# Kernel optimization log

Hardware: AMD Instinct MI355X
Metric: run time of the kernel (lower is better)

## Reference

```python
import jax, jax.numpy as jnp
import numpy as np

B, L, SH, EH, A, T = 128, 200, 512, 512, 512, 3


def setup_inputs() -> dict:
    key = jax.random.key(0)
    ks = jax.random.split(key, 13)
    s = 0.05  # small init scale to keep tanh/sigmoid unsaturated
    return {
        "sent_enc_doc": jax.random.normal(ks[0], (B, L, 2 * SH), jnp.float32),
        "h0_w": jax.random.normal(ks[1], (EH, SH), jnp.float32) * s,
        "h0_b": jax.random.normal(ks[2], (EH,), jnp.float32) * s,
        "gru_w_ih": jax.random.normal(ks[3], (3 * EH, 2 * SH), jnp.float32) * s,
        "gru_w_hh": jax.random.normal(ks[4], (3 * EH, EH), jnp.float32) * s,
        "gru_b_ih": jax.random.normal(ks[5], (3 * EH,), jnp.float32) * s,
        "gru_b_hh": jax.random.normal(ks[6], (3 * EH,), jnp.float32) * s,
        "wq": jax.random.normal(ks[7], (A, EH), jnp.float32) * s,
        "bq": jax.random.normal(ks[8], (A,), jnp.float32) * s,
        "wd": jax.random.normal(ks[9], (A, 2 * SH), jnp.float32) * s,
        "bd": jax.random.normal(ks[10], (A,), jnp.float32) * s,
        "ws": jax.random.normal(ks[11], (1, A), jnp.float32) * s,
        "bs": jax.random.normal(ks[12], (1,), jnp.float32) * s,
    }


def reference(sent_enc_doc, h0_w, h0_b, gru_w_ih, gru_w_hh, gru_b_ih, gru_b_hh,
              wq, bq, wd, bd, ws, bs):
    b, l, d2 = sent_enc_doc.shape
    sh = d2 // 2
    eh = gru_w_hh.shape[1]
    neg = jnp.asarray(-1e6, sent_enc_doc.dtype)

    # h0 = tanh(W * last backward vector), replicated across doc_len
    last_back = sent_enc_doc[:, 0, sh:]                      # (B, SH)
    h0 = jnp.tanh(last_back @ h0_w.T + h0_b)                 # (B, EH)
    h = jnp.broadcast_to(h0[:, None, :], (b, l, eh))         # (B, L, EH)

    s_prev = jnp.zeros((b, l, d2), sent_enc_doc.dtype)
    d_proj = sent_enc_doc @ wd.T + bd                        # (B, L, A) - loop-invariant
    mask = jnp.zeros((b, l), bool)
    rows = jnp.arange(b)

    scores_list, sel_list = [], []
    for _ in range(T):  # fixed, tiny, sequentially-dependent loop
        # GRUCell (torch gate order: r, z, n)
        gx = s_prev @ gru_w_ih.T + gru_b_ih                  # (B, L, 3EH)
        gh = h @ gru_w_hh.T + gru_b_hh                       # (B, L, 3EH)
        xr, xz, xn = jnp.split(gx, 3, axis=-1)
        hr, hz, hn = jnp.split(gh, 3, axis=-1)
        r = jax.nn.sigmoid(xr + hr)
        z = jax.nn.sigmoid(xz + hz)
        n = jnp.tanh(xn + r * hn)
        h = (1.0 - z) * n + z * h                            # (B, L, EH)

        # scorer: ws . tanh(Wq h + Wd s_i)
        score = (jnp.tanh(h @ wq.T + bq + d_proj) @ ws.T + bs)[..., 0]  # (B, L)
        score = jnp.where(mask, neg, score)
        idx = jnp.argmax(score, axis=1)                      # (B,)
        mask = mask.at[rows, idx].set(True)

        # gather the selected sentence encoding, broadcast to all positions
        s_sel = jnp.take_along_axis(sent_enc_doc, idx[:, None, None], axis=1)  # (B,1,2SH)
        s_prev = jnp.broadcast_to(s_sel, (b, l, d2))

        scores_list.append(score)
        sel_list.append(idx)

    sents_scores = jnp.stack(scores_list, axis=1)            # (B, T, L)
    sents_selected = jnp.stack(sel_list, axis=1)             # (B, T)
    return sents_scores, sents_selected
```

## Files before the change

kernel.cpp:

```cpp
#include <hip/hip_runtime.h>
#include <hip/hip_bf16.h>

constexpr int Bn  = 128;
constexpr int Ln  = 200;
constexpr int D2n = 1024;
constexpr int G3n = 1536;
constexpr int Tn  = 3;
constexpr int Nn  = 512;
constexpr int Kn  = 1024;

typedef unsigned short ushort;
typedef float f32x4 __attribute__((ext_vector_type(4)));
typedef __bf16 bf16x8 __attribute__((ext_vector_type(8)));

__device__ __forceinline__ ushort f2bf(float f) {
  unsigned u = __float_as_uint(f);
  unsigned r = (u + 0x7fffu + ((u >> 16) & 1u)) >> 16;
  return (ushort)r;
}
__device__ __forceinline__ float bf2f(ushort h) {
  return __uint_as_float(((unsigned)h) << 16);
}

__device__ __forceinline__ void gld_lds16(const ushort* g, ushort* l) {
  __builtin_amdgcn_global_load_lds(
      (const __attribute__((address_space(1))) unsigned int*)g,
      (__attribute__((address_space(3))) unsigned int*)l, 16, 0, 0);
}

__global__ void k_gather_lastb(const float* __restrict__ sent, float* __restrict__ lastb) {
  int i = blockIdx.x * 256 + threadIdx.x;
  int b = i >> 9, k = i & 511;
  lastb[i] = sent[(size_t)b * (Ln * D2n) + 512 + k];
}

__global__ void k_split(const float* __restrict__ W, ushort* __restrict__ hi,
                        ushort* __restrict__ lo) {
  int i = blockIdx.x * 256 + threadIdx.x;
  float4 v = ((const float4*)W)[i];
  ushort4 h, l;
  h.x = f2bf(v.x); l.x = f2bf(v.x - bf2f(h.x));
  h.y = f2bf(v.y); l.y = f2bf(v.y - bf2f(h.y));
  h.z = f2bf(v.z); l.z = f2bf(v.z - bf2f(h.z));
  h.w = f2bf(v.w); l.w = f2bf(v.w - bf2f(h.w));
  ((ushort4*)hi)[i] = h;
  ((ushort4*)lo)[i] = l;
}

template<int K, int ACT>
__launch_bounds__(256)
__global__ void k_small_gemm(const float* __restrict__ in, const float* __restrict__ W,
                             const float* __restrict__ bias, float* __restrict__ out, int J) {
  __shared__ float s[16 * K];
  const int b0 = blockIdx.y * 16;
  const int jl = threadIdx.x & 63;
  const int j  = blockIdx.x * 64 + jl;
  const int bg = (threadIdx.x >> 6) * 4;

  const float4* inp4 = (const float4*)(in + (size_t)b0 * K);
  float4* s4 = (float4*)s;
  for (int i = threadIdx.x; i < 4 * K; i += 256) s4[i] = inp4[i];
  __syncthreads();

  const float4* w4 = (const float4*)(W + (size_t)j * K);
  const float4* r0 = (const float4*)(s + (size_t)(bg + 0) * K);
  const float4* r1 = (const float4*)(s + (size_t)(bg + 1) * K);
  const float4* r2 = (const float4*)(s + (size_t)(bg + 2) * K);
  const float4* r3 = (const float4*)(s + (size_t)(bg + 3) * K);

  float acc0 = 0.f, acc1 = 0.f, acc2 = 0.f, acc3 = 0.f;
  #pragma unroll 4
  for (int k4 = 0; k4 < K / 4; ++k4) {
    float4 wv = w4[k4];
    float4 a;
    a = r0[k4]; acc0 += wv.x*a.x + wv.y*a.y + wv.z*a.z + wv.w*a.w;
    a = r1[k4]; acc1 += wv.x*a.x + wv.y*a.y + wv.z*a.z + wv.w*a.w;
    a = r2[k4]; acc2 += wv.x*a.x + wv.y*a.y + wv.z*a.z + wv.w*a.w;
    a = r3[k4]; acc3 += wv.x*a.x + wv.y*a.y + wv.z*a.z + wv.w*a.w;
  }
  float bb = bias[j];
  float v;
  v = acc0 + bb; if (ACT) v = tanhf(v); out[(size_t)(b0 + bg + 0) * J + j] = v;
  v = acc1 + bb; if (ACT) v = tanhf(v); out[(size_t)(b0 + bg + 1) * J + j] = v;
  v = acc2 + bb; if (ACT) v = tanhf(v); out[(size_t)(b0 + bg + 2) * J + j] = v;
  v = acc3 + bb; if (ACT) v = tanhf(v); out[(size_t)(b0 + bg + 3) * J + j] = v;
}

template<int KK>
__device__ __forceinline__ void mfma_tile128(
    const ushort* __restrict__ Ah, const ushort* __restrict__ Al,
    const ushort* __restrict__ Bh, const ushort* __restrict__ Bl,
    const float* __restrict__ bias, float* __restrict__ C, int ldc,
    int m0, int n0) {
  __shared__ __align__(16) ushort sAh[128 * 32];
  __shared__ __align__(16) ushort sAl[128 * 32];
  __shared__ __align__(16) ushort sBh[128 * 32];
  __shared__ __align__(16) ushort sBl[128 * 32];

  const int tid  = threadIdx.x;
  const int wave = tid >> 6, lane = tid & 63;
  const int wy = (wave >> 1) * 64, wx = (wave & 1) * 64;
  const int lm = lane & 15, lq = lane >> 4;
  const int fs = (lq ^ ((lm >> 1) & 3)) * 8;

  const int S0 = (wave * 2 + 0) * 64 + lane;
  const int S1 = (wave * 2 + 1) * 64 + lane;
  const int r0 = S0 >> 2, r1 = S1 >> 2;
  const int c0 = ((S0 & 3) ^ ((r0 >> 1) & 3)) * 8;
  const int c1 = ((S1 & 3) ^ ((r1 >> 1) & 3)) * 8;
  const ushort* pAh0 = Ah + (size_t)(m0 + r0) * KK + c0;
  const ushort* pAh1 = Ah + (size_t)(m0 + r1) * KK + c1;
  const ushort* pAl0 = Al + (size_t)(m0 + r0) * KK + c0;
  const ushort* pAl1 = Al + (size_t)(m0 + r1) * KK + c1;
  const ushort* pBh0 = Bh + (size_t)(n0 + r0) * KK + c0;
  const ushort* pBh1 = Bh + (size_t)(n0 + r1) * KK + c1;
  const ushort* pBl0 = Bl + (size_t)(n0 + r0) * KK + c0;
  const ushort* pBl1 = Bl + (size_t)(n0 + r1) * KK + c1;
  ushort* dA0 = &sAh[S0 * 8]; ushort* dA1 = &sAh[S1 * 8];
  ushort* dL0 = &sAl[S0 * 8]; ushort* dL1 = &sAl[S1 * 8];
  ushort* dB0 = &sBh[S0 * 8]; ushort* dB1 = &sBh[S1 * 8];
  ushort* dC0 = &sBl[S0 * 8]; ushort* dC1 = &sBl[S1 * 8];

  f32x4 acc[4][4] = {};

  for (int ks = 0; ks < KK / 32; ++ks) {
    const int ko = ks * 32;
    gld_lds16(pAh0 + ko, dA0); gld_lds16(pAh1 + ko, dA1);
    gld_lds16(pAl0 + ko, dL0); gld_lds16(pAl1 + ko, dL1);
    gld_lds16(pBh0 + ko, dB0); gld_lds16(pBh1 + ko, dB1);
    gld_lds16(pBl0 + ko, dC0); gld_lds16(pBl1 + ko, dC1);
    __syncthreads();

    bf16x8 ah[4], al[4], bh[4], bl[4];
    #pragma unroll
    for (int mi = 0; mi < 4; ++mi) {
      const int o = (wy + mi * 16 + lm) * 32 + fs;
      ah[mi] = *(const bf16x8*)&sAh[o];
      al[mi] = *(const bf16x8*)&sAl[o];
    }
    #pragma unroll
    for (int ni = 0; ni < 4; ++ni) {
      const int o = (wx + ni * 16 + lm) * 32 + fs;
      bh[ni] = *(const bf16x8*)&sBh[o];
      bl[ni] = *(const bf16x8*)&sBl[o];
    }
    #pragma unroll
    for (int mi = 0; mi < 4; ++mi)
      #pragma unroll
      for (int ni = 0; ni < 4; ++ni) {
        acc[mi][ni] = __builtin_amdgcn_mfma_f32_16x16x32_bf16(ah[mi], bh[ni], acc[mi][ni], 0, 0, 0);
        acc[mi][ni] = __builtin_amdgcn_mfma_f32_16x16x32_bf16(ah[mi], bl[ni], acc[mi][ni], 0, 0, 0);
        acc[mi][ni] = __builtin_amdgcn_mfma_f32_16x16x32_bf16(al[mi], bh[ni], acc[mi][ni], 0, 0, 0);
      }
    __syncthreads();
  }

  #pragma unroll
  for (int ni = 0; ni < 4; ++ni) {
    int col = n0 + wx + ni * 16 + lm;
    float bb = bias[col];
    #pragma unroll
    for (int mi = 0; mi < 4; ++mi) {
      int rbase = m0 + wy + mi * 16 + lq * 4;
      #pragma unroll
      for (int r = 0; r < 4; ++r)
        C[(size_t)(rbase + r) * ldc + col] = acc[mi][ni][r] + bb;
    }
  }
}

__launch_bounds__(256)
__global__ void k_dproj_mfma(const ushort* __restrict__ Ahi, const ushort* __restrict__ Alo,
                             const ushort* __restrict__ Whi, const ushort* __restrict__ Wlo,
                             const float* __restrict__ bias, float* __restrict__ C) {
  const int bid = blockIdx.x;
  mfma_tile128<1024>(Ahi, Alo, Whi, Wlo, bias, C, Nn, (bid % 200) * 128, (bid / 200) * 128);
}

__launch_bounds__(256)
__global__ void k_q_mfma(const ushort* __restrict__ hh, const ushort* __restrict__ hl,
                         const ushort* __restrict__ WqH, const ushort* __restrict__ WqL,
                         const float* __restrict__ bq, float* __restrict__ q) {
  mfma_tile128<512>(hh, hl, WqH, WqL, bq, q, 512, 0, blockIdx.x * 128);
}

__launch_bounds__(256)
__global__ void k_gates(const ushort* __restrict__ sxh, const ushort* __restrict__ sxl,
                        const float* __restrict__ hOld,
                        const ushort* __restrict__ hh, const ushort* __restrict__ hl,
                        const ushort* __restrict__ WihH, const ushort* __restrict__ WihL,
                        const ushort* __restrict__ WhhH, const ushort* __restrict__ WhhL,
                        const float* __restrict__ b_ih, const float* __restrict__ b_hh,
                        float* __restrict__ hNew, ushort* __restrict__ hhN,
                        ushort* __restrict__ hlN) {
  __shared__ __align__(16) ushort sAh[128 * 32];
  __shared__ __align__(16) ushort sAl[128 * 32];
  __shared__ __align__(16) ushort sWh[96 * 32];
  __shared__ __align__(16) ushort sWl[96 * 32];

  const int j0 = blockIdx.x * 32;
  const int tid = threadIdx.x, wave = tid >> 6, lane = tid & 63;
  const int wy = wave * 32;
  const int lm = lane & 15, lq = lane >> 4;
  const int fs = (lq ^ ((lm >> 1) & 3)) * 8;

  const int rA0 = tid >> 2;
  const int cA0 = ((tid & 3) ^ ((rA0 >> 1) & 3)) * 8;
  const int SA1 = tid + 256;
  const int rA1 = SA1 >> 2;
  const int cA1 = ((SA1 & 3) ^ ((rA1 >> 1) & 3)) * 8;
  const int gw0 = (rA0 >> 5) * 512 + j0 + (rA0 & 31);
  const int gw1 = (rA1 >> 5) * 512 + j0 + (rA1 & 31);
  const bool w1on = tid < 128;

  f32x4 ax[3][2][2] = {};
  f32x4 ag[3][2][2] = {};

  for (int ks = 0; ks < 32; ++ks) {
    const int ko = ks * 32;
    gld_lds16(sxh + (size_t)rA0 * 1024 + ko + cA0, &sAh[tid * 8]);
    gld_lds16(sxh + (size_t)rA1 * 1024 + ko + cA1, &sAh[SA1 * 8]);
    gld_lds16(sxl + (size_t)rA0 * 1024 + ko + cA0, &sAl[tid * 8]);
    gld_lds16(sxl + (size_t)rA1 * 1024 + ko + cA1, &sAl[SA1 * 8]);
    gld_lds16(WihH + (size_t)gw0 * 1024 + ko + cA0, &sWh[tid * 8]);
    gld_lds16(WihL + (size_t)gw0 * 1024 + ko + cA0, &sWl[tid * 8]);
    if (w1on) {
      gld_lds16(WihH + (size_t)gw1 * 1024 + ko + cA1, &sWh[SA1 * 8]);
      gld_lds16(WihL + (size_t)gw1 * 1024 + ko + cA1, &sWl[SA1 * 8]);
    }
    __syncthreads();

    bf16x8 fah[2], fal[2];
    #pragma unroll
    for (int mi = 0; mi < 2; ++mi) {
      const int o = (wy + mi * 16 + lm) * 32 + fs;
      fah[mi] = *(const bf16x8*)&sAh[o];
      fal[mi] = *(const bf16x8*)&sAl[o];
    }
    #pragma unroll
    for (int g = 0; g < 3; ++g)
      #pragma unroll
      for (int ni = 0; ni < 2; ++ni) {
        const int o = (g * 32 + ni * 16 + lm) * 32 + fs;
        bf16x8 fbh = *(const bf16x8*)&sWh[o];
        bf16x8 fbl = *(const bf16x8*)&sWl[o];
        #pragma unroll
        for (int mi = 0; mi < 2; ++mi) {
          ax[g][mi][ni] = __builtin_amdgcn_mfma_f32_16x16x32_bf16(fah[mi], fbh, ax[g][mi][ni], 0, 0, 0);
          ax[g][mi][ni] = __builtin_amdgcn_mfma_f32_16x16x32_bf16(fah[mi], fbl, ax[g][mi][ni], 0, 0, 0);
          ax[g][mi][ni] = __builtin_amdgcn_mfma_f32_16x16x32_bf16(fal[mi], fbh, ax[g][mi][ni], 0, 0, 0);
        }
      }
    __syncthreads();
  }

  for (int ks = 0; ks < 16; ++ks) {
    const int ko = ks * 32;
    gld_lds16(hh + (size_t)rA0 * 512 + ko + cA0, &sAh[tid * 8]);
    gld_lds16(hh + (size_t)rA1 * 512 + ko + cA1, &sAh[SA1 * 8]);
    gld_lds16(hl + (size_t)rA0 * 512 + ko + cA0, &sAl[tid * 8]);
    gld_lds16(hl + (size_t)rA1 * 512 + ko + cA1, &sAl[SA1 * 8]);
    gld_lds16(WhhH + (size_t)gw0 * 512 + ko + cA0, &sWh[tid * 8]);
    gld_lds16(WhhL + (size_t)gw0 * 512 + ko + cA0, &sWl[tid * 8]);
    if (w1on) {
      gld_lds16(WhhH + (size_t)gw1 * 512 + ko + cA1, &sWh[SA1 * 8]);
      gld_lds16(WhhL + (size_t)gw1 * 512 + ko + cA1, &sWl[SA1 * 8]);
    }
    __syncthreads();

    bf16x8 fah[2], fal[2];
    #pragma unroll
    for (int mi = 0; mi < 2; ++mi) {
      const int o = (wy + mi * 16 + lm) * 32 + fs;
      fah[mi] = *(const bf16x8*)&sAh[o];
      fal[mi] = *(const bf16x8*)&sAl[o];
    }
    #pragma unroll
    for (int g = 0; g < 3; ++g)
      #pragma unroll
      for (int ni = 0; ni < 2; ++ni) {
        const int o = (g * 32 + ni * 16 + lm) * 32 + fs;
        bf16x8 fbh = *(const bf16x8*)&sWh[o];
        bf16x8 fbl = *(const bf16x8*)&sWl[o];
        #pragma unroll
        for (int mi = 0; mi < 2; ++mi) {
          ag[g][mi][ni] = __builtin_amdgcn_mfma_f32_16x16x32_bf16(fah[mi], fbh, ag[g][mi][ni], 0, 0, 0);
          ag[g][mi][ni] = __builtin_amdgcn_mfma_f32_16x16x32_bf16(fah[mi], fbl, ag[g][mi][ni], 0, 0, 0);
          ag[g][mi][ni] = __builtin_amdgcn_mfma_f32_16x16x32_bf16(fal[mi], fbh, ag[g][mi][ni], 0, 0, 0);
        }
      }
    __syncthreads();
  }

  #pragma unroll
  for (int ni = 0; ni < 2; ++ni) {
    const int j = j0 + ni * 16 + lm;
    const float bir = b_ih[j], biz = b_ih[512 + j], bin = b_ih[1024 + j];
    const float bhr = b_hh[j], bhz = b_hh[512 + j], bhn = b_hh[1024 + j];
    #pragma unroll
    for (int mi = 0; mi < 2; ++mi) {
      const int rbase = wy + mi * 16 + lq * 4;
      #pragma unroll
      for (int rr = 0; rr < 4; ++rr) {
        const int b = rbase + rr;
        float xr = ax[0][mi][ni][rr] + bir, hr = ag[0][mi][ni][rr] + bhr;
        float xz = ax[1][mi][ni][rr] + biz, hz = ag[1][mi][ni][rr] + bhz;
        float xn = ax[2][mi][ni][rr] + bin, hn = ag[2][mi][ni][rr] + bhn;
        float r = 1.f / (1.f + expf(-(xr + hr)));
        float z = 1.f / (1.f + expf(-(xz + hz)));
        float n = tanhf(xn + r * hn);
        float hv = hOld[(size_t)b * 512 + j];
        float hw = (1.f - z) * n + z * hv;
        hNew[(size_t)b * 512 + j] = hw;
        ushort hbf = f2bf(hw);
        hhN[(size_t)b * 512 + j] = hbf;
        hlN[(size_t)b * 512 + j] = f2bf(hw - bf2f(hbf));
      }
    }
  }
}

__launch_bounds__(256)
__global__ void k_score(const float* __restrict__ dproj, const float* __restrict__ q,
                        const float* __restrict__ wsv, const float* __restrict__ bsv,
                        const int* __restrict__ mask, float* __restrict__ scoresf,
                        float* __restrict__ outScores, int t) {
  int w = blockIdx.x * 4 + (threadIdx.x >> 6);
  int lane = threadIdx.x & 63;
  int b = w / Ln, l = w % Ln;
  const float4* dp4 = (const float4*)(dproj + (size_t)w * Nn);
  const float4* q4  = (const float4*)(q + (size_t)b * Nn);
  const float4* ws4 = (const float4*)wsv;

  float sum = 0.f;
  #pragma unroll
  for (int i = 0; i < 2; ++i) {
    int idx = lane + i * 64;
    float4 d = dp4[idx], qq = q4[idx], wv = ws4[idx];
    sum += tanhf(qq.x + d.x) * wv.x + tanhf(qq.y + d.y) * wv.y
         + tanhf(qq.z + d.z) * wv.z + tanhf(qq.w + d.w) * wv.w;
  }
  #pragma unroll
  for (int off = 32; off > 0; off >>= 1) sum += __shfl_xor(sum, off, 64);

  if (lane == 0) {
    float v = sum + bsv[0];
    if (mask[w]) v = -1000000.0f;
    scoresf[w] = v;
    outScores[(size_t)b * (Tn * Ln) + t * Ln + l] = v;
  }
}

__launch_bounds__(256)
__global__ void k_argmax(const float* __restrict__ scoresf,
                         const float* __restrict__ sent,
                         ushort* __restrict__ s_rowh, ushort* __restrict__ s_rowl,
                         int* __restrict__ mask, float* __restrict__ outSel, int t) {
  int b = blockIdx.x;
  __shared__ int s_idx;
  int tid = threadIdx.x;
  if (tid < 64) {
    const float* sc = scoresf + (size_t)b * Ln;
    float best = -3.0e38f; int bi = 0;
    for (int l = tid; l < Ln; l += 64) {
      float v = sc[l];
      if (v > best) { best = v; bi = l; }
    }
    #pragma unroll
    for (int off = 32; off > 0; off >>= 1) {
      float ov = __shfl_down(best, off, 64);
      int   oi = __shfl_down(bi,   off, 64);
      if (ov > best || (ov == best && oi < bi)) { best = ov; bi = oi; }
    }
    if (tid == 0) s_idx = bi;
  }
  __syncthreads();
  int idx = s_idx;
  const float* src = sent + ((size_t)b * Ln + idx) * D2n;
  int k = tid * 4;
  float4 v = *(const float4*)(src + k);
  ushort4 hvec, lvec;
  hvec.x = f2bf(v.x); lvec.x = f2bf(v.x - bf2f(hvec.x));
  hvec.y = f2bf(v.y); lvec.y = f2bf(v.y - bf2f(hvec.y));
  hvec.z = f2bf(v.z); lvec.z = f2bf(v.z - bf2f(hvec.z));
  hvec.w = f2bf(v.w); lvec.w = f2bf(v.w - bf2f(hvec.w));
  *(ushort4*)(s_rowh + (size_t)b * 1024 + k) = hvec;
  *(ushort4*)(s_rowl + (size_t)b * 1024 + k) = lvec;
  if (tid == 0) {
    mask[b * Ln + idx] = 1;
    outSel[(size_t)b * Tn + t] = (float)idx;
  }
}

extern "C" void kernel_launch(void* const* d_in, const int* in_sizes, int n_in,
                              void* d_out, int out_size, void* d_ws, size_t ws_size,
                              hipStream_t stream) {
  const float* sent = (const float*)d_in[0];
  const float* h0_w = (const float*)d_in[1];
  const float* h0_b = (const float*)d_in[2];
  const float* w_ih = (const float*)d_in[3];
  const float* w_hh = (const float*)d_in[4];
  const float* b_ih = (const float*)d_in[5];
  const float* b_hh = (const float*)d_in[6];
  const float* wq   = (const float*)d_in[7];
  const float* bq   = (const float*)d_in[8];
  const float* wd   = (const float*)d_in[9];
  const float* bd   = (const float*)d_in[10];
  const float* wsv  = (const float*)d_in[11];
  const float* bsv  = (const float*)d_in[12];

  float* wsf     = (float*)d_ws;
  float* d_proj  = wsf;
  float* hA      = d_proj + 13107200;
  float* hB      = hA + 65536;
  float* lastb   = hB + 65536;
  float* q       = lastb + 65536;
  float* scoresf = q + 65536;
  int*   mask    = (int*)(scoresf + 25600);
  ushort* Whi    = (ushort*)(mask + 25600);
  ushort* Wlo    = Whi + 524288;
  ushort* Ahi    = Wlo + 524288;
  ushort* Alo    = Ahi + 26214400;

  ushort* WihH   = Ahi;
  ushort* WihL   = WihH + 1572864;
  ushort* WhhH   = WihL + 1572864;
  ushort* WhhL   = WhhH + 786432;
  ushort* WqH    = WhhL + 786432;
  ushort* WqL    = WqH + 262144;
  ushort* hhA    = WqL + 262144;
  ushort* hlA    = hhA + 65536;
  ushort* hhB    = hlA + 65536;
  ushort* hlB    = hhB + 65536;
  ushort* s_rowh = hlB + 65536;
  ushort* s_rowl = s_rowh + 131072;

  float* outScores = (float*)d_out;
  float* outSel    = outScores + (size_t)Bn * Tn * Ln;

  hipMemsetAsync(mask, 0, 25600 * sizeof(int), stream);

  k_gather_lastb<<<256, 256, 0, stream>>>(sent, lastb);
  k_small_gemm<512, 1><<<dim3(8, 8), 256, 0, stream>>>(lastb, h0_w, h0_b, hA, 512);
  k_split<<<512,   256, 0, stream>>>(wd, Whi, Wlo);
  k_split<<<25600, 256, 0, stream>>>(sent, Ahi, Alo);
  k_dproj_mfma<<<800, 256, 0, stream>>>(Ahi, Alo, Whi, Wlo, bd, d_proj);

  hipMemsetAsync(s_rowh, 0, 2 * 131072 * sizeof(ushort), stream);
  k_split<<<1536,  256, 0, stream>>>(w_ih, WihH, WihL);
  k_split<<<768,   256, 0, stream>>>(w_hh, WhhH, WhhL);
  k_split<<<256,   256, 0, stream>>>(wq, WqH, WqL);
  k_split<<<64,    256, 0, stream>>>(hA, hhA, hlA);

  float* hc = hA;  ushort* hhc = hhA; ushort* hlc = hlA;
  float* hn = hB;  ushort* hhn = hhB; ushort* hln = hlB;
  for (int t = 0; t < Tn; ++t) {
    k_gates<<<16, 256, 0, stream>>>(s_rowh, s_rowl, hc, hhc, hlc,
                                    WihH, WihL, WhhH, WhhL, b_ih, b_hh,
                                    hn, hhn, hln);
    k_q_mfma<<<4, 256, 0, stream>>>(hhn, hln, WqH, WqL, bq, q);
    k_score<<<6400, 256, 0, stream>>>(d_proj, q, wsv, bsv, mask, scoresf, outScores, t);
    k_argmax<<<128, 256, 0, stream>>>(scoresf, sent, s_rowh, s_rowl, mask, outSel, t);
    float* tf = hc; hc = hn; hn = tf;
    ushort* t1 = hhc; hhc = hhn; hhn = t1;
    ushort* t2 = hlc; hlc = hln; hln = t2;
  }
}
```

Measured before the change: 592.6 us.

## Fuse score+argmax, h0 gather+split, weight splits; retile gates over 64 blocks

Several changes land together. The last-backward gather is merged into the h0 GEMM, which now also writes the bf16 hi/lo split. The three weight splits become one launch. The GRU gates kernel is retiled from 16 blocks to 64 blocks of 64 rows x 16 columns, with a two-slice K stage per sync. Score and argmax are fused into one per-batch kernel that keeps scores in LDS and uses a fast exp-based tanh. The aim is fewer launches, better CU occupancy in the gates kernel and no scores round trip through global memory, but the fused score kernel runs only 128 blocks, which may cut parallelism on the d_proj read.

Measured after the change: 570.0 us. 3.8% less time.

```diff
diff --git a/kernel.cpp b/kernel.cpp
--- a/kernel.cpp
+++ b/kernel.cpp
@@ -28,10 +28,10 @@
       (__attribute__((address_space(3))) unsigned int*)l, 16, 0, 0);
 }
 
-__global__ void k_gather_lastb(const float* __restrict__ sent, float* __restrict__ lastb) {
-  int i = blockIdx.x * 256 + threadIdx.x;
-  int b = i >> 9, k = i & 511;
-  lastb[i] = sent[(size_t)b * (Ln * D2n) + 512 + k];
+__device__ __forceinline__ float ftanh(float x) {
+  float cx = fminf(fmaxf(x, -15.f), 15.f);
+  float e  = __expf(2.f * cx);
+  return (e - 1.f) * __builtin_amdgcn_rcpf(e + 1.f);
 }
 
 __global__ void k_split(const float* __restrict__ W, ushort* __restrict__ hi,
@@ -47,30 +47,51 @@
   ((ushort4*)lo)[i] = l;
 }
 
-template<int K, int ACT>
+__global__ void k_split3(const float* __restrict__ w_ih, const float* __restrict__ w_hh,
+                         const float* __restrict__ wq,
+                         ushort* __restrict__ WihH, ushort* __restrict__ WihL,
+                         ushort* __restrict__ WhhH, ushort* __restrict__ WhhL,
+                         ushort* __restrict__ WqH, ushort* __restrict__ WqL) {
+  int i = blockIdx.x * 256 + threadIdx.x;
+  const float* src; ushort* hi; ushort* lo; int off;
+  if (i < 393216)      { src = w_ih; hi = WihH; lo = WihL; off = i; }
+  else if (i < 589824) { src = w_hh; hi = WhhH; lo = WhhL; off = i - 393216; }
+  else                 { src = wq;   hi = WqH;  lo = WqL;  off = i - 589824; }
+  float4 v = ((const float4*)src)[off];
+  ushort4 h, l;
+  h.x = f2bf(v.x); l.x = f2bf(v.x - bf2f(h.x));
+  h.y = f2bf(v.y); l.y = f2bf(v.y - bf2f(h.y));
+  h.z = f2bf(v.z); l.z = f2bf(v.z - bf2f(h.z));
+  h.w = f2bf(v.w); l.w = f2bf(v.w - bf2f(h.w));
+  ((ushort4*)hi)[off] = h;
+  ((ushort4*)lo)[off] = l;
+}
+
 __launch_bounds__(256)
-__global__ void k_small_gemm(const float* __restrict__ in, const float* __restrict__ W,
-                             const float* __restrict__ bias, float* __restrict__ out, int J) {
-  __shared__ float s[16 * K];
+__global__ void k_h0(const float* __restrict__ sent, const float* __restrict__ W,
+                     const float* __restrict__ bias, float* __restrict__ out,
+                     ushort* __restrict__ outh, ushort* __restrict__ outl) {
+  __shared__ float s[16 * 512];
   const int b0 = blockIdx.y * 16;
   const int jl = threadIdx.x & 63;
   const int j  = blockIdx.x * 64 + jl;
   const int bg = (threadIdx.x >> 6) * 4;
 
-  const float4* inp4 = (const float4*)(in + (size_t)b0 * K);
-  float4* s4 = (float4*)s;
-  for (int i = threadIdx.x; i < 4 * K; i += 256) s4[i] = inp4[i];
+  for (int i = threadIdx.x; i < 2048; i += 256) {
+    int r = i >> 7, c = i & 127;
+    ((float4*)s)[i] = *(const float4*)(sent + (size_t)(b0 + r) * (Ln * D2n) + 512 + c * 4);
+  }
   __syncthreads();
 
-  const float4* w4 = (const float4*)(W + (size_t)j * K);
-  const float4* r0 = (const float4*)(s + (size_t)(bg + 0) * K);
-  const float4* r1 = (const float4*)(s + (size_t)(bg + 1) * K);
-  const float4* r2 = (const float4*)(s + (size_t)(bg + 2) * K);
-  const float4* r3 = (const float4*)(s + (size_t)(bg + 3) * K);
+  const float4* w4 = (const float4*)(W + (size_t)j * 512);
+  const float4* r0 = (const float4*)(s + (size_t)(bg + 0) * 512);
+  const float4* r1 = (const float4*)(s + (size_t)(bg + 1) * 512);
+  const float4* r2 = (const float4*)(s + (size_t)(bg + 2) * 512);
+  const float4* r3 = (const float4*)(s + (size_t)(bg + 3) * 512);
 
   float acc0 = 0.f, acc1 = 0.f, acc2 = 0.f, acc3 = 0.f;
   #pragma unroll 4
-  for (int k4 = 0; k4 < K / 4; ++k4) {
+  for (int k4 = 0; k4 < 128; ++k4) {
     float4 wv = w4[k4];
     float4 a;
     a = r0[k4]; acc0 += wv.x*a.x + wv.y*a.y + wv.z*a.z + wv.w*a.w;
@@ -79,11 +100,16 @@
     a = r3[k4]; acc3 += wv.x*a.x + wv.y*a.y + wv.z*a.z + wv.w*a.w;
   }
   float bb = bias[j];
-  float v;
-  v = acc0 + bb; if (ACT) v = tanhf(v); out[(size_t)(b0 + bg + 0) * J + j] = v;
-  v = acc1 + bb; if (ACT) v = tanhf(v); out[(size_t)(b0 + bg + 1) * J + j] = v;
-  v = acc2 + bb; if (ACT) v = tanhf(v); out[(size_t)(b0 + bg + 2) * J + j] = v;
-  v = acc3 + bb; if (ACT) v = tanhf(v); out[(size_t)(b0 + bg + 3) * J + j] = v;
+  float accs[4] = {acc0, acc1, acc2, acc3};
+  #pragma unroll
+  for (int i = 0; i < 4; ++i) {
+    float v = tanhf(accs[i] + bb);
+    size_t o = (size_t)(b0 + bg + i) * 512 + j;
+    out[o] = v;
+    ushort hv = f2bf(v);
+    outh[o] = hv;
+    outl[o] = f2bf(v - bf2f(hv));
+  }
 }
 
 template<int KK>
@@ -193,177 +219,148 @@
                         const float* __restrict__ b_ih, const float* __restrict__ b_hh,
                         float* __restrict__ hNew, ushort* __restrict__ hhN,
                         ushort* __restrict__ hlN) {
-  __shared__ __align__(16) ushort sAh[128 * 32];
-  __shared__ __align__(16) ushort sAl[128 * 32];
-  __shared__ __align__(16) ushort sWh[96 * 32];
-  __shared__ __align__(16) ushort sWl[96 * 32];
-
-  const int j0 = blockIdx.x * 32;
+  __shared__ __align__(16) ushort sAh[2][64 * 32];
+  __shared__ __align__(16) ushort sAl[2][64 * 32];
+  __shared__ __align__(16) ushort sWh[2][48 * 32];
+  __shared__ __align__(16) ushort sWl[2][48 * 32];
+
+  const int bb  = blockIdx.x >> 5;
+  const int j0  = (blockIdx.x & 31) * 16;
+  const int rb0 = bb * 64;
   const int tid = threadIdx.x, wave = tid >> 6, lane = tid & 63;
-  const int wy = wave * 32;
+  const int wy = wave * 16;
   const int lm = lane & 15, lq = lane >> 4;
   const int fs = (lq ^ ((lm >> 1) & 3)) * 8;
 
-  const int rA0 = tid >> 2;
-  const int cA0 = ((tid & 3) ^ ((rA0 >> 1) & 3)) * 8;
-  const int SA1 = tid + 256;
-  const int rA1 = SA1 >> 2;
-  const int cA1 = ((SA1 & 3) ^ ((rA1 >> 1) & 3)) * 8;
-  const int gw0 = (rA0 >> 5) * 512 + j0 + (rA0 & 31);
-  const int gw1 = (rA1 >> 5) * 512 + j0 + (rA1 & 31);
-  const bool w1on = tid < 128;
-
-  f32x4 ax[3][2][2] = {};
-  f32x4 ag[3][2][2] = {};
-
-  for (int ks = 0; ks < 32; ++ks) {
-    const int ko = ks * 32;
-    gld_lds16(sxh + (size_t)rA0 * 1024 + ko + cA0, &sAh[tid * 8]);
-    gld_lds16(sxh + (size_t)rA1 * 1024 + ko + cA1, &sAh[SA1 * 8]);
-    gld_lds16(sxl + (size_t)rA0 * 1024 + ko + cA0, &sAl[tid * 8]);
-    gld_lds16(sxl + (size_t)rA1 * 1024 + ko + cA1, &sAl[SA1 * 8]);
-    gld_lds16(WihH + (size_t)gw0 * 1024 + ko + cA0, &sWh[tid * 8]);
-    gld_lds16(WihL + (size_t)gw0 * 1024 + ko + cA0, &sWl[tid * 8]);
-    if (w1on) {
-      gld_lds16(WihH + (size_t)gw1 * 1024 + ko + cA1, &sWh[SA1 * 8]);
-      gld_lds16(WihL + (size_t)gw1 * 1024 + ko + cA1, &sWl[SA1 * 8]);
-    }
-    __syncthreads();
-
-    bf16x8 fah[2], fal[2];
-    #pragma unroll
-    for (int mi = 0; mi < 2; ++mi) {
-      const int o = (wy + mi * 16 + lm) * 32 + fs;
-      fah[mi] = *(const bf16x8*)&sAh[o];
-      fal[mi] = *(const bf16x8*)&sAl[o];
-    }
-    #pragma unroll
-    for (int g = 0; g < 3; ++g)
+  const int rA = tid >> 2;
+  const int cA = ((tid & 3) ^ ((rA >> 1) & 3)) * 8;
+  const bool wOn = tid < 192;
+  const int gw = (rA >> 4) * 512 + j0 + (rA & 15);
+
+  f32x4 ax[3] = {};
+  f32x4 ag[3] = {};
+
+  for (int ks = 0; ks < 16; ++ks) {
+    const int ko = ks * 64;
+    #pragma unroll
+    for (int kk = 0; kk < 2; ++kk) {
+      gld_lds16(sxh + (size_t)(rb0 + rA) * 1024 + ko + kk * 32 + cA, &sAh[kk][tid * 8]);
+      gld_lds16(sxl + (size_t)(rb0 + rA) * 1024 + ko + kk * 32 + cA, &sAl[kk][tid * 8]);
+      if (wOn) {
+        gld_lds16(WihH + (size_t)gw * 1024 + ko + kk * 32 + cA, &sWh[kk][tid * 8]);
+        gld_lds16(WihL + (size_t)gw * 1024 + ko + kk * 32 + cA, &sWl[kk][tid * 8]);
+      }
+    }
+    __syncthreads();
+    #pragma unroll
+    for (int kk = 0; kk < 2; ++kk) {
+      const int oA = (wy + lm) * 32 + fs;
+      bf16x8 fah = *(const bf16x8*)&sAh[kk][oA];
+      bf16x8 fal = *(const bf16x8*)&sAl[kk][oA];
       #pragma unroll
-      for (int ni = 0; ni < 2; ++ni) {
-        const int o = (g * 32 + ni * 16 + lm) * 32 + fs;
-        bf16x8 fbh = *(const bf16x8*)&sWh[o];
-        bf16x8 fbl = *(const bf16x8*)&sWl[o];
-        #pragma unroll
-        for (int mi = 0; mi < 2; ++mi) {
-          ax[g][mi][ni] = __builtin_amdgcn_mfma_f32_16x16x32_bf16(fah[mi], fbh, ax[g][mi][ni], 0, 0, 0);
-          ax[g][mi][ni] = __builtin_amdgcn_mfma_f32_16x16x32_bf16(fah[mi], fbl, ax[g][mi][ni], 0, 0, 0);
-          ax[g][mi][ni] = __builtin_amdgcn_mfma_f32_16x16x32_bf16(fal[mi], fbh, ax[g][mi][ni], 0, 0, 0);
-        }
+      for (int g = 0; g < 3; ++g) {
+        const int oW = (g * 16 + lm) * 32 + fs;
+        bf16x8 fbh = *(const bf16x8*)&sWh[kk][oW];
+        bf16x8 fbl = *(const bf16x8*)&sWl[kk][oW];
+        ax[g] = __builtin_amdgcn_mfma_f32_16x16x32_bf16(fah, fbh, ax[g], 0, 0, 0);
+        ax[g] = __builtin_amdgcn_mfma_f32_16x16x32_bf16(fah, fbl, ax[g], 0, 0, 0);
+        ax[g] = __builtin_amdgcn_mfma_f32_16x16x32_bf16(fal, fbh, ax[g], 0, 0, 0);
       }
-    __syncthreads();
-  }
-
-  for (int ks = 0; ks < 16; ++ks) {
-    const int ko = ks * 32;
-    gld_lds16(hh + (size_t)rA0 * 512 + ko + cA0, &sAh[tid * 8]);
-    gld_lds16(hh + (size_t)rA1 * 512 + ko + cA1, &sAh[SA1 * 8]);
-    gld_lds16(hl + (size_t)rA0 * 512 + ko + cA0, &sAl[tid * 8]);
-    gld_lds16(hl + (size_t)rA1 * 512 + ko + cA1, &sAl[SA1 * 8]);
-    gld_lds16(WhhH + (size_t)gw0 * 512 + ko + cA0, &sWh[tid * 8]);
-    gld_lds16(WhhL + (size_t)gw0 * 512 + ko + cA0, &sWl[tid * 8]);
-    if (w1on) {
-      gld_lds16(WhhH + (size_t)gw1 * 512 + ko + cA1, &sWh[SA1 * 8]);
-      gld_lds16(WhhL + (size_t)gw1 * 512 + ko + cA1, &sWl[SA1 * 8]);
-    }
-    __syncthreads();
-
-    bf16x8 fah[2], fal[2];
-    #pragma unroll
-    for (int mi = 0; mi < 2; ++mi) {
-      const int o = (wy + mi * 16 + lm) * 32 + fs;
-      fah[mi] = *(const bf16x8*)&sAh[o];
-      fal[mi] = *(const bf16x8*)&sAl[o];
-    }
-    #pragma unroll
-    for (int g = 0; g < 3; ++g)
+    }
+    __syncthreads();
+  }
+
+  for (int ks = 0; ks < 8; ++ks) {
+    const int ko = ks * 64;
+    #pragma unroll
+    for (int kk = 0; kk < 2; ++kk) {
+      gld_lds16(hh + (size_t)(rb0 + rA) * 512 + ko + kk * 32 + cA, &sAh[kk][tid * 8]);
+      gld_lds16(hl + (size_t)(rb0 + rA) * 512 + ko + kk * 32 + cA, &sAl[kk][tid * 8]);
+      if (wOn) {
+        gld_lds16(WhhH + (size_t)gw * 512 + ko + kk * 32 + cA, &sWh[kk][tid * 8]);
+        gld_lds16(WhhL + (size_t)gw * 512 + ko + kk * 32 + cA, &sWl[kk][tid * 8]);
+      }
+    }
+    __syncthreads();
+    #pragma unroll
+    for (int kk = 0; kk < 2; ++kk) {
+      const int oA = (wy + lm) * 32 + fs;
+      bf16x8 fah = *(const bf16x8*)&sAh[kk][oA];
+      bf16x8 fal = *(const bf16x8*)&sAl[kk][oA];
       #pragma unroll
-      for (int ni = 0; ni < 2; ++ni) {
-        const int o = (g * 32 + ni * 16 + lm) * 32 + fs;
-        bf16x8 fbh = *(const bf16x8*)&sWh[o];
-        bf16x8 fbl = *(const bf16x8*)&sWl[o];
-        #pragma unroll
-        for (int mi = 0; mi < 2; ++mi) {
-          ag[g][mi][ni] = __builtin_amdgcn_mfma_f32_16x16x32_bf16(fah[mi], fbh, ag[g][mi][ni], 0, 0, 0);
-          ag[g][mi][ni] = __builtin_amdgcn_mfma_f32_16x16x32_bf16(fah[mi], fbl, ag[g][mi][ni], 0, 0, 0);
-          ag[g][mi][ni] = __builtin_amdgcn_mfma_f32_16x16x32_bf16(fal[mi], fbh, ag[g][mi][ni], 0, 0, 0);
-        }
+      for (int g = 0; g < 3; ++g) {
+        const int oW = (g * 16 + lm) * 32 + fs;
+        bf16x8 fbh = *(const bf16x8*)&sWh[kk][oW];
+        bf16x8 fbl = *(const bf16x8*)&sWl[kk][oW];
+        ag[g] = __builtin_amdgcn_mfma_f32_16x16x32_bf16(fah, fbh, ag[g], 0, 0, 0);
+        ag[g] = __builtin_amdgcn_mfma_f32_16x16x32_bf16(fah, fbl, ag[g], 0, 0, 0);
+        ag[g] = __builtin_amdgcn_mfma_f32_16x16x32_bf16(fal, fbh, ag[g], 0, 0, 0);
       }
-    __syncthreads();
-  }
-
+    }
+    __syncthreads();
+  }
+
+  const int j = j0 + lm;
+  const float bir = b_ih[j], biz = b_ih[512 + j], bin = b_ih[1024 + j];
+  const float bhr = b_hh[j], bhz = b_hh[512 + j], bhn = b_hh[1024 + j];
   #pragma unroll
-  for (int ni = 0; ni < 2; ++ni) {
-    const int j = j0 + ni * 16 + lm;
-    const float bir = b_ih[j], biz = b_ih[512 + j], bin = b_ih[1024 + j];
-    const float bhr = b_hh[j], bhz = b_hh[512 + j], bhn = b_hh[1024 + j];
-    #pragma unroll
-    for (int mi = 0; mi < 2; ++mi) {
-      const int rbase = wy + mi * 16 + lq * 4;
-      #pragma unroll
-      for (int rr = 0; rr < 4; ++rr) {
-        const int b = rbase + rr;
-        float xr = ax[0][mi][ni][rr] + bir, hr = ag[0][mi][ni][rr] + bhr;
-        float xz = ax[1][mi][ni][rr] + biz, hz = ag[1][mi][ni][rr] + bhz;
-        float xn = ax[2][mi][ni][rr] + bin, hn = ag[2][mi][ni][rr] + bhn;
-        float r = 1.f / (1.f + expf(-(xr + hr)));
-        float z = 1.f / (1.f + expf(-(xz + hz)));
-        float n = tanhf(xn + r * hn);
-        float hv = hOld[(size_t)b * 512 + j];
-        float hw = (1.f - z) * n + z * hv;
-        hNew[(size_t)b * 512 + j] = hw;
-        ushort hbf = f2bf(hw);
-        hhN[(size_t)b * 512 + j] = hbf;
-        hlN[(size_t)b * 512 + j] = f2bf(hw - bf2f(hbf));
-      }
-    }
+  for (int rr = 0; rr < 4; ++rr) {
+    const int b = rb0 + wy + lq * 4 + rr;
+    float xr = ax[0][rr] + bir, hr = ag[0][rr] + bhr;
+    float xz = ax[1][rr] + biz, hz = ag[1][rr] + bhz;
+    float xn = ax[2][rr] + bin, hn = ag[2][rr] + bhn;
+    float r = 1.f / (1.f + expf(-(xr + hr)));
+    float z = 1.f / (1.f + expf(-(xz + hz)));
+    float n = tanhf(xn + r * hn);
+    float hv = hOld[(size_t)b * 512 + j];
+    float hw = (1.f - z) * n + z * hv;
+    hNew[(size_t)b * 512 + j] = hw;
+    ushort hbf = f2bf(hw);
+    hhN[(size_t)b * 512 + j] = hbf;
+    hlN[(size_t)b * 512 + j] = f2bf(hw - bf2f(hbf));
   }
 }
 
 __launch_bounds__(256)
-__global__ void k_score(const float* __restrict__ dproj, const float* __restrict__ q,
-                        const float* __restrict__ wsv, const float* __restrict__ bsv,
-                        const int* __restrict__ mask, float* __restrict__ scoresf,
-                        float* __restrict__ outScores, int t) {
-  int w = blockIdx.x * 4 + (threadIdx.x >> 6);
-  int lane = threadIdx.x & 63;
-  int b = w / Ln, l = w % Ln;
-  const float4* dp4 = (const float4*)(dproj + (size_t)w * Nn);
+__global__ void k_score_argmax(const float* __restrict__ dproj, const float* __restrict__ q,
+                               const float* __restrict__ wsv, const float* __restrict__ bsv,
+                               const float* __restrict__ sent,
+                               ushort* __restrict__ s_rowh, ushort* __restrict__ s_rowl,
+                               int* __restrict__ mask, float* __restrict__ outScores,
+                               float* __restrict__ outSel, int t) {
+  const int b = blockIdx.x;
+  const int tid = threadIdx.x, lane = tid & 63, wv = tid >> 6;
+  __shared__ float ssc[Ln];
+  __shared__ int s_idx;
+
   const float4* q4  = (const float4*)(q + (size_t)b * Nn);
   const float4* ws4 = (const float4*)wsv;
-
-  float sum = 0.f;
-  #pragma unroll
-  for (int i = 0; i < 2; ++i) {
-    int idx = lane + i * 64;
-    float4 d = dp4[idx], qq = q4[idx], wv = ws4[idx];
-    sum += tanhf(qq.x + d.x) * wv.x + tanhf(qq.y + d.y) * wv.y
-         + tanhf(qq.z + d.z) * wv.z + tanhf(qq.w + d.w) * wv.w;
-  }
-  #pragma unroll
-  for (int off = 32; off > 0; off >>= 1) sum += __shfl_xor(sum, off, 64);
-
-  if (lane == 0) {
-    float v = sum + bsv[0];
-    if (mask[w]) v = -1000000.0f;
-    scoresf[w] = v;
-    outScores[(size_t)b * (Tn * Ln) + t * Ln + l] = v;
-  }
-}
-
-__launch_bounds__(256)
-__global__ void k_argmax(const float* __restrict__ scoresf,
-                         const float* __restrict__ sent,
-                         ushort* __restrict__ s_rowh, ushort* __restrict__ s_rowl,
-                         int* __restrict__ mask, float* __restrict__ outSel, int t) {
-  int b = blockIdx.x;
-  __shared__ int s_idx;
-  int tid = threadIdx.x;
+  const float4 qq0 = q4[lane],  qq1 = q4[lane + 64];
+  const float4 wv0 = ws4[lane], wv1 = ws4[lane + 64];
+  const float bs0 = bsv[0];
+
+  for (int l = wv; l < Ln; l += 4) {
+    const float4* dp4 = (const float4*)(dproj + ((size_t)b * Ln + l) * Nn);
+    float4 d0 = dp4[lane], d1 = dp4[lane + 64];
+    float sum = ftanh(qq0.x + d0.x) * wv0.x + ftanh(qq0.y + d0.y) * wv0.y
+              + ftanh(qq0.z + d0.z) * wv0.z + ftanh(qq0.w + d0.w) * wv0.w
+              + ftanh(qq1.x + d1.x) * wv1.x + ftanh(qq1.y + d1.y) * wv1.y
+              + ftanh(qq1.z + d1.z) * wv1.z + ftanh(qq1.w + d1.w) * wv1.w;
+    #pragma unroll
+    for (int off = 32; off > 0; off >>= 1) sum += __shfl_xor(sum, off, 64);
+    if (lane == 0) {
+      float v = sum + bs0;
+      if (mask[b * Ln + l]) v = -1000000.0f;
+      ssc[l] = v;
+      outScores[(size_t)b * (Tn * Ln) + t * Ln + l] = v;
+    }
+  }
+  __syncthreads();
+
   if (tid < 64) {
-    const float* sc = scoresf + (size_t)b * Ln;
     float best = -3.0e38f; int bi = 0;
     for (int l = tid; l < Ln; l += 64) {
-      float v = sc[l];
+      float v = ssc[l];
       if (v > best) { best = v; bi = l; }
     }
     #pragma unroll
@@ -413,13 +410,17 @@
   float* d_proj  = wsf;
   float* hA      = d_proj + 13107200;
   float* hB      = hA + 65536;
-  float* lastb   = hB + 65536;
-  float* q       = lastb + 65536;
-  float* scoresf = q + 65536;
-  int*   mask    = (int*)(scoresf + 25600);
+  float* q       = hB + 65536;
+  int*   mask    = (int*)(q + 65536);
   ushort* Whi    = (ushort*)(mask + 25600);
   ushort* Wlo    = Whi + 524288;
-  ushort* Ahi    = Wlo + 524288;
+  ushort* hhA    = Wlo + 524288;
+  ushort* hlA    = hhA + 65536;
+  ushort* hhB    = hlA + 65536;
+  ushort* hlB    = hhB + 65536;
+  ushort* s_rowh = hlB + 65536;
+  ushort* s_rowl = s_rowh + 131072;
+  ushort* Ahi    = s_rowl + 131072;
   ushort* Alo    = Ahi + 26214400;
 
   ushort* WihH   = Ahi;
@@ -428,39 +429,29 @@
   ushort* WhhL   = WhhH + 786432;
   ushort* WqH    = WhhL + 786432;
   ushort* WqL    = WqH + 262144;
-  ushort* hhA    = WqL + 262144;
-  ushort* hlA    = hhA + 65536;
-  ushort* hhB    = hlA + 65536;
-  ushort* hlB    = hhB + 65536;
-  ushort* s_rowh = hlB + 65536;
-  ushort* s_rowl = s_rowh + 131072;
 
   float* outScores = (float*)d_out;
   float* outSel    = outScores + (size_t)Bn * Tn * Ln;
 
   hipMemsetAsync(mask, 0, 25600 * sizeof(int), stream);
-
-  k_gather_lastb<<<256, 256, 0, stream>>>(sent, lastb);
-  k_small_gemm<512, 1><<<dim3(8, 8), 256, 0, stream>>>(lastb, h0_w, h0_b, hA, 512);
+  hipMemsetAsync(s_rowh, 0, 2 * 131072 * sizeof(ushort), stream);
+
+  k_h0<<<dim3(8, 8), 256, 0, stream>>>(sent, h0_w, h0_b, hA, hhA, hlA);
   k_split<<<512,   256, 0, stream>>>(wd, Whi, Wlo);
   k_split<<<25600, 256, 0, stream>>>(sent, Ahi, Alo);
   k_dproj_mfma<<<800, 256, 0, stream>>>(Ahi, Alo, Whi, Wlo, bd, d_proj);
-
-  hipMemsetAsync(s_rowh, 0, 2 * 131072 * sizeof(ushort), stream);
-  k_split<<<1536,  256, 0, stream>>>(w_ih, WihH, WihL);
-  k_split<<<768,   256, 0, stream>>>(w_hh, WhhH, WhhL);
-  k_split<<<256,   256, 0, stream>>>(wq, WqH, WqL);
-  k_split<<<64,    256, 0, stream>>>(hA, hhA, hlA);
+  k_split3<<<2560, 256, 0, stream>>>(w_ih, w_hh, wq, WihH, WihL, WhhH, WhhL, WqH, WqL);
 
   float* hc = hA;  ushort* hhc = hhA; ushort* hlc = hlA;
   float* hn = hB;  ushort* hhn = hhB; ushort* hln = hlB;
   for (int t = 0; t < Tn; ++t) {
-    k_gates<<<16, 256, 0, stream>>>(s_rowh, s_rowl, hc, hhc, hlc,
+    k_gates<<<64, 256, 0, stream>>>(s_rowh, s_rowl, hc, hhc, hlc,
                                     WihH, WihL, WhhH, WhhL, b_ih, b_hh,
                                     hn, hhn, hln);
     k_q_mfma<<<4, 256, 0, stream>>>(hhn, hln, WqH, WqL, bq, q);
-    k_score<<<6400, 256, 0, stream>>>(d_proj, q, wsv, bsv, mask, scoresf, outScores, t);
-    k_argmax<<<128, 256, 0, stream>>>(scoresf, sent, s_rowh, s_rowl, mask, outSel, t);
+    k_score_argmax<<<128, 256, 0, stream>>>(d_proj, q, wsv, bsv, sent,
+                                            s_rowh, s_rowl, mask,
+                                            outScores, outSel, t);
     float* tf = hc; hc = hn; hn = tf;
     ushort* t1 = hhc; hhc = hhn; hhn = t1;
     ushort* t2 = hlc; hlc = hln; hln = t2;
```
